# Kernel tuning notes

Measured on AMD Instinct MI355X. Metric: run time of the kernel, lower is better.

## Reference

```python
import jax, jax.numpy as jnp
import numpy as np

N_RAYS = 65536
N_SAMPLES = 4194304  # ~64 samples per ray, packed
D = 8


def setup_inputs() -> dict:
    key = jax.random.key(0)
    k1, k2 = jax.random.split(key)
    sample_values = jax.random.normal(k1, (N_SAMPLES, D), dtype=jnp.float32)
    ray_indices = jnp.sort(jax.random.randint(k2, (N_SAMPLES,), 0, N_RAYS, dtype=jnp.int32))
    return {"sample_values": sample_values, "ray_indices": ray_indices, "n_rays": N_RAYS}


def reference(sample_values, ray_indices, n_rays):
    # Segment-sum over variable-length per-ray sample packs.
    values_sum_per_ray = jax.ops.segment_sum(
        sample_values, ray_indices, num_segments=n_rays, indices_are_sorted=True
    )  # [n_rays, D]
    # Each sample receives its ray's total sum (gather back).
    values_sum_per_sample = values_sum_per_ray[ray_indices]  # [n_samples, D]
    return (values_sum_per_ray, values_sum_per_sample)
```

## Files before the change

kernel.cpp:

```cpp
#include <hip/hip_runtime.h>


#define DCH 8

__global__ void __launch_bounds__(256) bounds_kernel(
    const int* __restrict__ rays,
    int* __restrict__ seg_start,
    int* __restrict__ seg_end,
    int n_samples) {
  long i = (long)blockIdx.x * blockDim.x + threadIdx.x;
  if (i >= n_samples) return;
  int r = rays[i];
  if (i == 0 || rays[i - 1] != r) seg_start[r] = (int)i;
  if (i == n_samples - 1 || rays[i + 1] != r) seg_end[r] = (int)(i + 1);
}

__global__ void __launch_bounds__(256) raysum_kernel(
    const float2* __restrict__ vals2,
    const int* __restrict__ seg_start,
    const int* __restrict__ seg_end,
    float* __restrict__ out_ray,
    float2* __restrict__ out_sample2,
    int n_rays) {
  int wave = blockIdx.x * (blockDim.x >> 6) + (threadIdx.x >> 6);
  if (wave >= n_rays) return;
  const int lane = threadIdx.x & 63;
  const int sl = lane >> 2;
  const int ch2 = lane & 3;

  const int s0 = seg_start[wave];
  const int s1 = (s0 >= 0) ? seg_end[wave] : 0;

  float2 acc = {0.f, 0.f};
  if (s0 >= 0) {
    for (int j = s0 + sl; j < s1; j += 16) {
      float2 v = vals2[(long)j * 4 + ch2];
      acc.x += v.x;
      acc.y += v.y;
    }
  }

#pragma unroll
  for (int off = 4; off <= 32; off <<= 1) {
    acc.x += __shfl_xor(acc.x, off, 64);
    acc.y += __shfl_xor(acc.y, off, 64);
  }

  if (lane < 4) {
    *reinterpret_cast<float2*>(out_ray + (long)wave * DCH + 2 * lane) = acc;
  }

  if (s0 >= 0) {
    for (int j = s0 + sl; j < s1; j += 16) {
      out_sample2[(long)j * 4 + ch2] = acc;
    }
  }
}

extern "C" void kernel_launch(void* const* d_in, const int* in_sizes, int n_in,
                              void* d_out, int out_size, void* d_ws, size_t ws_size,
                              hipStream_t stream) {
  const float* vals = (const float*)d_in[0];
  const int* rays   = (const int*)d_in[1];

  const int n_samples = in_sizes[1];
  const int d         = in_sizes[0] / n_samples;
  const int n_rays    = out_size / d - n_samples;

  float* out_ray    = (float*)d_out;
  float* out_sample = out_ray + (size_t)n_rays * d;

  int* seg_start = (int*)d_ws;
  int* seg_end   = seg_start + n_rays;

  (void)hipMemsetAsync(seg_start, 0xFF, (size_t)2 * n_rays * sizeof(int), stream);

  bounds_kernel<<<(int)(((long)n_samples + 255) / 256), 256, 0, stream>>>(
      rays, seg_start, seg_end, n_samples);

  const int nblocks = (n_rays + 3) / 4;
  raysum_kernel<<<nblocks, 256, 0, stream>>>(
      reinterpret_cast<const float2*>(vals), seg_start, seg_end,
      out_ray, reinterpret_cast<float2*>(out_sample), n_rays);
}
```

Before: 264.7 us.

## Process eight rays per wave with 16-byte loads and drop the memset

The bounds kernel now fills empty-ray gaps itself, so the hipMemsetAsync of the segment arrays is removed. The raysum kernel gives each wave eight rays, loading their bounds once and broadcasting them with shuffles. Values are read and written as 16-byte float4 vectors, and per-sample outputs use nontemporal stores. This cuts launch and per-wave overhead and widens memory transactions, at the cost of processing each wave's rays serially and running long gap-fill loops in the bounds kernel when ray gaps are large.

Measured after the change: 274.0 us. 1.03x slower.

```diff
diff --git a/kernel.cpp b/kernel.cpp
--- a/kernel.cpp
+++ b/kernel.cpp
@@ -2,57 +2,82 @@
 
 
 #define DCH 8
+#define RPW 8
+
+typedef float f32x4 __attribute__((ext_vector_type(4)));
 
 __global__ void __launch_bounds__(256) bounds_kernel(
     const int* __restrict__ rays,
     int* __restrict__ seg_start,
     int* __restrict__ seg_end,
-    int n_samples) {
+    int n_samples, int n_rays) {
   long i = (long)blockIdx.x * blockDim.x + threadIdx.x;
   if (i >= n_samples) return;
   int r = rays[i];
-  if (i == 0 || rays[i - 1] != r) seg_start[r] = (int)i;
-  if (i == n_samples - 1 || rays[i + 1] != r) seg_end[r] = (int)(i + 1);
+  if (i == 0) {
+    seg_start[r] = 0;
+    for (int g = 0; g < r; ++g) { seg_start[g] = 0; seg_end[g] = 0; }
+  } else {
+    int rp = rays[i - 1];
+    if (rp != r) {
+      seg_end[rp] = (int)i;
+      seg_start[r] = (int)i;
+      for (int g = rp + 1; g < r; ++g) { seg_start[g] = (int)i; seg_end[g] = (int)i; }
+    }
+  }
+  if (i == n_samples - 1) {
+    seg_end[r] = n_samples;
+    for (int g = r + 1; g < n_rays; ++g) { seg_start[g] = n_samples; seg_end[g] = n_samples; }
+  }
 }
 
 __global__ void __launch_bounds__(256) raysum_kernel(
-    const float2* __restrict__ vals2,
+    const f32x4* __restrict__ vals4,
     const int* __restrict__ seg_start,
     const int* __restrict__ seg_end,
-    float* __restrict__ out_ray,
-    float2* __restrict__ out_sample2,
+    f32x4* __restrict__ out_ray4,
+    f32x4* __restrict__ out_sample4,
     int n_rays) {
-  int wave = blockIdx.x * (blockDim.x >> 6) + (threadIdx.x >> 6);
-  if (wave >= n_rays) return;
+  const int wave = blockIdx.x * (blockDim.x >> 6) + (threadIdx.x >> 6);
+  const int base = wave * RPW;
+  if (base >= n_rays) return;
   const int lane = threadIdx.x & 63;
-  const int sl = lane >> 2;
-  const int ch2 = lane & 3;
+  const int sl = lane >> 1;
+  const int h = lane & 1;
 
-  const int s0 = seg_start[wave];
-  const int s1 = (s0 >= 0) ? seg_end[wave] : 0;
-
-  float2 acc = {0.f, 0.f};
-  if (s0 >= 0) {
-    for (int j = s0 + sl; j < s1; j += 16) {
-      float2 v = vals2[(long)j * 4 + ch2];
-      acc.x += v.x;
-      acc.y += v.y;
-    }
+  const int ridx = base + (lane & (RPW - 1));
+  int rs = 0, re = 0;
+  if (ridx < n_rays) {
+    rs = seg_start[ridx];
+    re = seg_end[ridx];
   }
 
+#pragma unroll 1
+  for (int r = 0; r < RPW; ++r) {
+    if (base + r >= n_rays) break;
+    const int s0 = __shfl(rs, r, 64);
+    const int s1 = __shfl(re, r, 64);
+
+    f32x4 acc = {0.f, 0.f, 0.f, 0.f};
+    for (int j = s0 + sl; j < s1; j += 32) {
+      f32x4 v = vals4[(long)j * 2 + h];
+      acc += v;
+    }
+
 #pragma unroll
-  for (int off = 4; off <= 32; off <<= 1) {
-    acc.x += __shfl_xor(acc.x, off, 64);
-    acc.y += __shfl_xor(acc.y, off, 64);
-  }
+    for (int off = 2; off <= 32; off <<= 1) {
+      acc.x += __shfl_xor(acc.x, off, 64);
+      acc.y += __shfl_xor(acc.y, off, 64);
+      acc.z += __shfl_xor(acc.z, off, 64);
+      acc.w += __shfl_xor(acc.w, off, 64);
+    }
 
-  if (lane < 4) {
-    *reinterpret_cast<float2*>(out_ray + (long)wave * DCH + 2 * lane) = acc;
-  }
+    if (lane < 2) {
+      out_ray4[(long)(base + r) * 2 + lane] = acc;
+    }
 
-  if (s0 >= 0) {
-    for (int j = s0 + sl; j < s1; j += 16) {
-      out_sample2[(long)j * 4 + ch2] = acc;
+    for (int j = s0 + sl; j < s1; j += 32) {
+      __builtin_nontemporal_store(acc, &out_sample4[(long)j * 2 + h]);
     }
   }
 }
@@ -73,13 +98,13 @@
   int* seg_start = (int*)d_ws;
   int* seg_end   = seg_start + n_rays;
 
-  (void)hipMemsetAsync(seg_start, 0xFF, (size_t)2 * n_rays * sizeof(int), stream);
+  bounds_kernel<<<(int)(((long)n_samples + 255) / 256), 256, 0, stream>>>(
+      rays, seg_start, seg_end, n_samples, n_rays);
 
-  bounds_kernel<<<(int)(((long)n_samples + 255) / 256), 256, 0, stream>>>(
-      rays, seg_start, seg_end, n_samples);
-
-  const int nblocks = (n_rays + 3) / 4;
+  const int nwaves = (n_rays + RPW - 1) / RPW;
+  const int nblocks = (nwaves + 3) / 4;
   raysum_kernel<<<nblocks, 256, 0, stream>>>(
-      reinterpret_cast<const float2*>(vals), seg_start, seg_end,
-      out_ray, reinterpret_cast<float2*>(out_sample), n_rays);
+      reinterpret_cast<const f32x4*>(vals), seg_start, seg_end,
+      reinterpret_cast<f32x4*>(out_ray),
+      reinterpret_cast<f32x4*>(out_sample), n_rays);
 }
```
